# Kernel optimization log

Hardware: AMD Instinct MI355X
Metric: run time of the kernel (lower is better)

## Reference

```python
import jax, jax.numpy as jnp
import numpy as np

N_NODES = 100000
N_EDGES = 1600000
IN_DIM = 256
HEADS = 4
OUT_DIM = 32
NEG_SLOPE = 0.2


def setup_inputs() -> dict:
    key = jax.random.key(0)
    ks = jax.random.split(key, 6)
    x = jax.random.normal(ks[0], (N_NODES, IN_DIM), dtype=jnp.float32)
    # xavier-ish init scale for fc and attention vectors
    W = jax.random.normal(ks[1], (IN_DIM, HEADS * OUT_DIM), dtype=jnp.float32) * (1.0 / np.sqrt(IN_DIM))
    attn_l = jax.random.normal(ks[2], (HEADS, OUT_DIM), dtype=jnp.float32) * (1.0 / np.sqrt(OUT_DIM))
    attn_r = jax.random.normal(ks[3], (HEADS, OUT_DIM), dtype=jnp.float32) * (1.0 / np.sqrt(OUT_DIM))
    src = jax.random.randint(ks[4], (N_EDGES,), 0, N_NODES, dtype=jnp.int32)
    dst = jax.random.randint(ks[5], (N_EDGES,), 0, N_NODES, dtype=jnp.int32)
    return {"x": x, "W": W, "attn_l": attn_l, "attn_r": attn_r, "src": src, "dst": dst}


def reference(x, W, attn_l, attn_r, src, dst):
    N = x.shape[0]
    H, D = attn_l.shape
    # shared linear projection (feat_drop = 0)
    feat = (x @ W).reshape(N, H, D)                      # [N,H,D]
    el = jnp.sum(feat * attn_l, axis=-1)                 # [N,H]
    er = jnp.sum(feat * attn_r, axis=-1)                 # [N,H]
    e = jax.nn.leaky_relu(el[src] + er[dst], NEG_SLOPE)  # [E,H]
    # edge softmax over incoming edges of each destination node
    m = jax.ops.segment_max(e, dst, num_segments=N)      # [N,H]
    m = jnp.where(jnp.isfinite(m), m, 0.0)               # zero-in-degree guard
    ex = jnp.exp(e - m[dst])                             # [E,H]
    denom = jax.ops.segment_sum(ex, dst, num_segments=N) # [N,H]
    a = ex / jnp.maximum(denom[dst], 1e-9)               # [E,H] (attn_drop = 0)
    # weighted scatter-add aggregation
    out = jax.ops.segment_sum(a[:, :, None] * feat[src], dst, num_segments=N)  # [N,H,D]
    # head mean (the .mean(1) in GAT1.forward)
    return out.mean(axis=1)                              # [N,D]
```

## Files before the change

### kernel.cpp

```cpp
#include <hip/hip_runtime.h>
#include <math.h>

#define NN 100000
#define NE 1600000
#define IN_DIM 256
#define HD 128
#define NEG_SLOPE 0.2f

#define B1SH 9
#define NPB (1 << B1SH)
#define NB1 ((NN + NPB - 1) / NPB)
#define SC_BLOCKS ((NE / 4 + 1023) / 1024)

typedef __attribute__((ext_vector_type(8))) __bf16 bf16x8;
typedef __attribute__((ext_vector_type(4))) float floatx4;

__device__ inline unsigned short f2bf(float f) {
    unsigned int b = __float_as_uint(f);
    b += 0x7fffu + ((b >> 16) & 1u);
    return (unsigned short)(b >> 16);
}
__device__ inline unsigned int pk(float lo, float hi) {
    return (unsigned int)f2bf(lo) | ((unsigned int)f2bf(hi) << 16);
}
__device__ inline float bflo(unsigned int u) { return __uint_as_float(u << 16); }
__device__ inline float bfhi(unsigned int u) { return __uint_as_float(u & 0xffff0000u); }
__device__ inline float lrelu(float v) { return (v > 0.f) ? v : v * NEG_SLOPE; }

__global__ __launch_bounds__(256) void prep_w_kernel(const float* __restrict__ W,
                                                     unsigned int* __restrict__ wswz) {
    int g = blockIdx.x * 256 + threadIdx.x;
    int lane = g & 63;
    int t = (g >> 6) & 7;
    int c = g >> 9;
    int sub = lane & 15, quad = lane >> 4;
    int n = t * 16 + sub;
    int kbase = c * 32 + quad * 8;
    unsigned int ob = (unsigned int)g * 4;
#pragma unroll
    for (int i = 0; i < 4; ++i) {
        float lo = W[(size_t)(kbase + 2 * i) * HD + n];
        float hi = W[(size_t)(kbase + 2 * i + 1) * HD + n];
        wswz[ob + i] = pk(lo, hi);
    }
}

__global__ __launch_bounds__(256, 4) void gemm_kernel(const float* __restrict__ x,
                                                      const uint4* __restrict__ wswz,
                                                      const float* __restrict__ attn_l,
                                                      const float* __restrict__ attn_r,
                                                      unsigned short* __restrict__ featb,
                                                      float* __restrict__ el,
                                                      float* __restrict__ er) {
    const int tid = threadIdx.x;
    const int lane = tid & 63, wv = tid >> 6;
    const int sub = lane & 15, quad = lane >> 4;
    const int row0 = blockIdx.x * 64 + wv * 16;

    int m = row0 + sub;
    if (m >= NN) m = NN - 1;
    const float* xp = x + (size_t)m * IN_DIM + quad * 8;

    bf16x8 af[8];
#pragma unroll
    for (int h = 0; h < 2; ++h) {
        float4 raw[4][2];
#pragma unroll
        for (int c = 0; c < 4; ++c) {
            raw[c][0] = *(const float4*)(xp + (h * 4 + c) * 32);
            raw[c][1] = *(const float4*)(xp + (h * 4 + c) * 32 + 4);
        }
#pragma unroll
        for (int c = 0; c < 4; ++c) {
            uint4 au;
            au.x = pk(raw[c][0].x, raw[c][0].y);
            au.y = pk(raw[c][0].z, raw[c][0].w);
            au.z = pk(raw[c][1].x, raw[c][1].y);
            au.w = pk(raw[c][1].z, raw[c][1].w);
            af[h * 4 + c] = __builtin_bit_cast(bf16x8, au);
        }
    }

    floatx4 acc[8];
#pragma unroll
    for (int t = 0; t < 8; ++t) acc[t] = (floatx4){0.f, 0.f, 0.f, 0.f};

#pragma unroll
    for (int c = 0; c < 8; ++c) {
        uint4 bu[8];
#pragma unroll
        for (int t = 0; t < 8; ++t) bu[t] = wswz[(c * 8 + t) * 64 + lane];
#pragma unroll
        for (int t = 0; t < 8; ++t) {
            bf16x8 bfr = __builtin_bit_cast(bf16x8, bu[t]);
            acc[t] = __builtin_amdgcn_mfma_f32_16x16x32_bf16(af[c], bfr, acc[t], 0, 0, 0);
        }
    }

    float al[8], ar[8];
#pragma unroll
    for (int t = 0; t < 8; ++t) {
        al[t] = attn_l[t * 16 + sub];
        ar[t] = attn_r[t * 16 + sub];
    }

#pragma unroll
    for (int r = 0; r < 4; ++r) {
        int row = row0 + quad * 4 + r;
        uint4 fv;
        fv.x = pk(acc[0][r], acc[1][r]);
        fv.y = pk(acc[2][r], acc[3][r]);
        fv.z = pk(acc[4][r], acc[5][r]);
        fv.w = pk(acc[6][r], acc[7][r]);
        float pl[4], pr[4];
#pragma unroll
        for (int hh = 0; hh < 4; ++hh) {
            pl[hh] = acc[2 * hh][r] * al[2 * hh] + acc[2 * hh + 1][r] * al[2 * hh + 1];
            pr[hh] = acc[2 * hh][r] * ar[2 * hh] + acc[2 * hh + 1][r] * ar[2 * hh + 1];
        }
#pragma unroll
        for (int o = 1; o < 16; o <<= 1) {
#pragma unroll
            for (int hh = 0; hh < 4; ++hh) {
                pl[hh] += __shfl_xor(pl[hh], o);
                pr[hh] += __shfl_xor(pr[hh], o);
            }
        }
        if (row < NN) {
            *(uint4*)(featb + (size_t)row * HD + sub * 8) = fv;
            if (sub < 4) {
                float vl = (sub == 0) ? pl[0] : (sub == 1) ? pl[1] : (sub == 2) ? pl[2] : pl[3];
                float vr = (sub == 0) ? pr[0] : (sub == 1) ? pr[1] : (sub == 2) ? pr[2] : pr[3];
                el[row * 4 + sub] = vl;
                er[row * 4 + sub] = vr;
            }
        }
    }
}

__global__ __launch_bounds__(256) void precount_kernel(const int4* __restrict__ dst4,
                                                       int* __restrict__ gbcnt) {
    __shared__ int cnt[NB1];
    int t = threadIdx.x;
    for (int i = t; i < NB1; i += 256) cnt[i] = 0;
    __syncthreads();
    int base4 = blockIdx.x * 1024;
#pragma unroll
    for (int k = 0; k < 4; ++k) {
        int gi = base4 + k * 256 + t;
        if (gi < NE / 4) {
            int4 d = dst4[gi];
            atomicAdd(&cnt[d.x >> B1SH], 1);
            atomicAdd(&cnt[d.y >> B1SH], 1);
            atomicAdd(&cnt[d.z >> B1SH], 1);
            atomicAdd(&cnt[d.w >> B1SH], 1);
        }
    }
    __syncthreads();
    for (int i = t; i < NB1; i += 256)
        if (cnt[i]) atomicAdd(&gbcnt[i], cnt[i]);
}

__global__ __launch_bounds__(256) void bscan_kernel(const int* __restrict__ gbcnt,
                                                    int* __restrict__ regstart,
                                                    int* __restrict__ gcursor,
                                                    int* __restrict__ offs) {
    __shared__ int sh[256];
    int t = threadIdx.x;
    int v = (t < NB1) ? gbcnt[t] : 0;
    sh[t] = v;
    __syncthreads();
    for (int o = 1; o < 256; o <<= 1) {
        int a = (t >= o) ? sh[t - o] : 0;
        __syncthreads();
        sh[t] += a;
        __syncthreads();
    }
    int excl = sh[t] - v;
    if (t < NB1) {
        regstart[t] = excl;
        gcursor[t] = excl;
    }
    if (t == 0) {
        regstart[NB1] = NE;
        offs[NN] = NE;
    }
}

__global__ __launch_bounds__(256) void scatter_kernel(const int4* __restrict__ src4,
                                                      const int4* __restrict__ dst4,
                                                      int* __restrict__ gcursor,
                                                      unsigned int* __restrict__ pkd) {
    __shared__ int cnt[NB1];
    __shared__ int gbase[NB1];
    int t = threadIdx.x;
    for (int i = t; i < NB1; i += 256) cnt[i] = 0;
    __syncthreads();

    int base4 = blockIdx.x * 1024;
    unsigned int pkv[16];
    unsigned int brk[16];
#pragma unroll
    for (int k = 0; k < 4; ++k) {
        int gi = base4 + k * 256 + t;
        bool ok = gi < NE / 4;
        int gic = ok ? gi : 0;
        int4 s = src4[gic];
        int4 d = dst4[gic];
        int dd[4] = {d.x, d.y, d.z, d.w};
        int ss[4] = {s.x, s.y, s.z, s.w};
#pragma unroll
        for (int j4 = 0; j4 < 4; ++j4) {
            int e = k * 4 + j4;
            if (ok) {
                int b = dd[j4] >> B1SH;
                int r = atomicAdd(&cnt[b], 1);
                brk[e] = ((unsigned int)b << 12) | (unsigned int)r;
                pkv[e] = ((unsigned int)(dd[j4] & (NPB - 1)) << 17) | (unsigned int)ss[j4];
            } else {
                brk[e] = 0xFFFFFFFFu;
            }
        }
    }
    __syncthreads();
    for (int i = t; i < NB1; i += 256)
        gbase[i] = cnt[i] ? atomicAdd(&gcursor[i], cnt[i]) : 0;
    __syncthreads();
#pragma unroll
    for (int e = 0; e < 16; ++e) {
        if (brk[e] != 0xFFFFFFFFu) {
            int b = brk[e] >> 12;
            int r = brk[e] & 0xFFF;
            pkd[gbase[b] + r] = pkv[e];
        }
    }
}

__global__ __launch_bounds__(256) void build_kernel(const unsigned int* __restrict__ pkd,
                                                    const int* __restrict__ regstart,
                                                    int* __restrict__ offs,
                                                    int* __restrict__ csr_src) {
    __shared__ int fcnt[NPB];
    __shared__ int foffs[NPB];
    __shared__ int ssc[256];
    int b = blockIdx.x, t = threadIdx.x;
    int rs = regstart[b], re = regstart[b + 1];
    int n = re - rs;

    for (int i = t; i < NPB; i += 256) fcnt[i] = 0;
    __syncthreads();
    for (int i = t; i < n; i += 256) {
        unsigned int v = pkd[rs + i];
        atomicAdd(&fcnt[v >> 17], 1);
    }
    __syncthreads();
    int a0 = fcnt[2 * t], a1 = fcnt[2 * t + 1];
    int s = a0 + a1;
    ssc[t] = s;
    __syncthreads();
    for (int o = 1; o < 256; o <<= 1) {
        int u = (t >= o) ? ssc[t - o] : 0;
        __syncthreads();
        ssc[t] += u;
        __syncthreads();
    }
    int excl = ssc[t] - s;
    foffs[2 * t] = excl;
    foffs[2 * t + 1] = excl + a0;
    __syncthreads();
#pragma unroll
    for (int q = 0; q < 2; ++q) {
        int j = t + q * 256;
        int node = b * NPB + j;
        if (node < NN) offs[node] = rs + foffs[j];
    }
    for (int i = t; i < NPB; i += 256) fcnt[i] = 0;
    __syncthreads();
    int i = t;
    for (; i + 768 < n; i += 1024) {
        unsigned int v0 = pkd[rs + i];
        unsigned int v1 = pkd[rs + i + 256];
        unsigned int v2 = pkd[rs + i + 512];
        unsigned int v3 = pkd[rs + i + 768];
        int j0 = v0 >> 17, j1 = v1 >> 17, j2 = v2 >> 17, j3 = v3 >> 17;
        int r0 = atomicAdd(&fcnt[j0], 1);
        int r1 = atomicAdd(&fcnt[j1], 1);
        int r2 = atomicAdd(&fcnt[j2], 1);
        int r3 = atomicAdd(&fcnt[j3], 1);
        csr_src[rs + foffs[j0] + r0] = (int)(v0 & 0x1FFFFu);
        csr_src[rs + foffs[j1] + r1] = (int)(v1 & 0x1FFFFu);
        csr_src[rs + foffs[j2] + r2] = (int)(v2 & 0x1FFFFu);
        csr_src[rs + foffs[j3] + r3] = (int)(v3 & 0x1FFFFu);
    }
    for (; i < n; i += 256) {
        unsigned int v = pkd[rs + i];
        int j = v >> 17;
        int r = atomicAdd(&fcnt[j], 1);
        csr_src[rs + foffs[j] + r] = (int)(v & 0x1FFFFu);
    }
}

#define CH 32
__global__ __launch_bounds__(256) void aggregate_kernel(const uint4* __restrict__ featu4,
                                                        const float4* __restrict__ el4,
                                                        const float4* __restrict__ er4,
                                                        const int* __restrict__ offs,
                                                        const int* __restrict__ csr_src,
                                                        float* __restrict__ out) {
    __shared__ int    s_sv[4][4][CH];
    __shared__ float4 s_a4[4][4][CH];

    const int tid = threadIdx.x;
    const int lane = tid & 63, wv = tid >> 6;
    const int g = lane >> 4, sub = lane & 15;
    const int node = blockIdx.x * 16 + wv * 4 + g;
    const int beg = offs[node], end = offs[node + 1];

    const float4 erv = er4[node];
    float4 sm = make_float4(0.f, 0.f, 0.f, 0.f);
    float acc[8];
#pragma unroll
    for (int i = 0; i < 8; ++i) acc[i] = 0.f;

    for (int c0 = beg; c0 < end; c0 += CH) {
        int cnt = end - c0;
        if (cnt > CH) cnt = CH;
#pragma unroll
        for (int t = 0; t < 2; ++t) {
            int slot = sub + t * 16;
            if (slot < cnt) {
                int s = csr_src[c0 + slot];
                float4 e = el4[s];
                float4 w;
                w.x = __expf(lrelu(e.x + erv.x));
                w.y = __expf(lrelu(e.y + erv.y));
                w.z = __expf(lrelu(e.z + erv.z));
                w.w = __expf(lrelu(e.w + erv.w));
                sm.x += w.x; sm.y += w.y; sm.z += w.z; sm.w += w.w;
                s_sv[wv][g][slot] = s;
                s_a4[wv][g][slot] = w;
            }
        }
        int j = 0;
        for (; j + 4 <= cnt; j += 4) {
            int s0 = s_sv[wv][g][j + 0];
            int s1 = s_sv[wv][g][j + 1];
            int s2 = s_sv[wv][g][j + 2];
            int s3 = s_sv[wv][g][j + 3];
            uint4 u0 = featu4[(size_t)s0 * 16 + sub];
            uint4 u1 = featu4[(size_t)s1 * 16 + sub];
            uint4 u2 = featu4[(size_t)s2 * 16 + sub];
            uint4 u3 = featu4[(size_t)s3 * 16 + sub];
            float4 w0 = s_a4[wv][g][j + 0];
            float4 w1 = s_a4[wv][g][j + 1];
            float4 w2 = s_a4[wv][g][j + 2];
            float4 w3 = s_a4[wv][g][j + 3];
            acc[0] = fmaf(w0.x, bflo(u0.x), acc[0]); acc[1] = fmaf(w0.x, bfhi(u0.x), acc[1]);
            acc[2] = fmaf(w0.y, bflo(u0.y), acc[2]); acc[3] = fmaf(w0.y, bfhi(u0.y), acc[3]);
            acc[4] = fmaf(w0.z, bflo(u0.z), acc[4]); acc[5] = fmaf(w0.z, bfhi(u0.z), acc[5]);
            acc[6] = fmaf(w0.w, bflo(u0.w), acc[6]); acc[7] = fmaf(w0.w, bfhi(u0.w), acc[7]);
            acc[0] = fmaf(w1.x, bflo(u1.x), acc[0]); acc[1] = fmaf(w1.x, bfhi(u1.x), acc[1]);
            acc[2] = fmaf(w1.y, bflo(u1.y), acc[2]); acc[3] = fmaf(w1.y, bfhi(u1.y), acc[3]);
            acc[4] = fmaf(w1.z, bflo(u1.z), acc[4]); acc[5] = fmaf(w1.z, bfhi(u1.z), acc[5]);
            acc[6] = fmaf(w1.w, bflo(u1.w), acc[6]); acc[7] = fmaf(w1.w, bfhi(u1.w), acc[7]);
            acc[0] = fmaf(w2.x, bflo(u2.x), acc[0]); acc[1] = fmaf(w2.x, bfhi(u2.x), acc[1]);
            acc[2] = fmaf(w2.y, bflo(u2.y), acc[2]); acc[3] = fmaf(w2.y, bfhi(u2.y), acc[3]);
            acc[4] = fmaf(w2.z, bflo(u2.z), acc[4]); acc[5] = fmaf(w2.z, bfhi(u2.z), acc[5]);
            acc[6] = fmaf(w2.w, bflo(u2.w), acc[6]); acc[7] = fmaf(w2.w, bfhi(u2.w), acc[7]);
            acc[0] = fmaf(w3.x, bflo(u3.x), acc[0]); acc[1] = fmaf(w3.x, bfhi(u3.x), acc[1]);
            acc[2] = fmaf(w3.y, bflo(u3.y), acc[2]); acc[3] = fmaf(w3.y, bfhi(u3.y), acc[3]);
            acc[4] = fmaf(w3.z, bflo(u3.z), acc[4]); acc[5] = fmaf(w3.z, bfhi(u3.z), acc[5]);
            acc[6] = fmaf(w3.w, bflo(u3.w), acc[6]); acc[7] = fmaf(w3.w, bfhi(u3.w), acc[7]);
        }
        for (; j < cnt; ++j) {
            int s = s_sv[wv][g][j];
            uint4 u = featu4[(size_t)s * 16 + sub];
            float4 w = s_a4[wv][g][j];
            acc[0] = fmaf(w.x, bflo(u.x), acc[0]); acc[1] = fmaf(w.x, bfhi(u.x), acc[1]);
            acc[2] = fmaf(w.y, bflo(u.y), acc[2]); acc[3] = fmaf(w.y, bfhi(u.y), acc[3]);
            acc[4] = fmaf(w.z, bflo(u.z), acc[4]); acc[5] = fmaf(w.z, bfhi(u.z), acc[5]);
            acc[6] = fmaf(w.w, bflo(u.w), acc[6]); acc[7] = fmaf(w.w, bfhi(u.w), acc[7]);
        }
    }

#pragma unroll
    for (int o = 1; o < 16; o <<= 1) {
        sm.x += __shfl_xor(sm.x, o);
        sm.y += __shfl_xor(sm.y, o);
        sm.z += __shfl_xor(sm.z, o);
        sm.w += __shfl_xor(sm.w, o);
    }
    float ix = 1.f / fmaxf(sm.x, 1e-9f);
    float iy = 1.f / fmaxf(sm.y, 1e-9f);
    float iz = 1.f / fmaxf(sm.z, 1e-9f);
    float iw = 1.f / fmaxf(sm.w, 1e-9f);
    float ox = 0.25f * (acc[0] * ix + acc[2] * iy + acc[4] * iz + acc[6] * iw);
    float oy = 0.25f * (acc[1] * ix + acc[3] * iy + acc[5] * iz + acc[7] * iw);
    out[node * 32 + sub]      = ox;
    out[node * 32 + 16 + sub] = oy;
}

extern "C" void kernel_launch(void* const* d_in, const int* in_sizes, int n_in,
                              void* d_out, int out_size, void* d_ws, size_t ws_size,
                              hipStream_t stream) {
    const float* x      = (const float*)d_in[0];
    const float* W      = (const float*)d_in[1];
    const float* attn_l = (const float*)d_in[2];
    const float* attn_r = (const float*)d_in[3];
    const int*   src    = (const int*)d_in[4];
    const int*   dst    = (const int*)d_in[5];
    float* out = (float*)d_out;

    char* p = (char*)d_ws;
    auto alloc = [&](size_t bytes) -> void* {
        void* r = (void*)p;
        p += (bytes + 255) & ~(size_t)255;
        return r;
    };
    unsigned short* featb = (unsigned short*)alloc((size_t)NN * HD * 2);
    unsigned int*   wswz  = (unsigned int*)alloc(4096 * 16);
    float* el      = (float*)alloc((size_t)NN * 4 * 4);
    float* er      = (float*)alloc((size_t)NN * 4 * 4);
    int*   offs    = (int*)alloc((size_t)(NN + 1) * 4);
    unsigned int* pkd = (unsigned int*)alloc((size_t)NE * 4);
    int*   csr     = (int*)alloc((size_t)NE * 4);
    int*   gbcnt   = (int*)alloc((size_t)NB1 * 4);
    int*   regstart= (int*)alloc((size_t)(NB1 + 1) * 4);
    int*   gcursor = (int*)alloc((size_t)NB1 * 4);

    hipMemsetAsync(gbcnt, 0, (size_t)NB1 * 4, stream);

    prep_w_kernel<<<16, 256, 0, stream>>>(W, wswz);
    gemm_kernel<<<(NN + 63) / 64, 256, 0, stream>>>(x, (const uint4*)wswz, attn_l, attn_r,
                                                    featb, el, er);
    precount_kernel<<<SC_BLOCKS, 256, 0, stream>>>((const int4*)dst, gbcnt);
    bscan_kernel<<<1, 256, 0, stream>>>(gbcnt, regstart, gcursor, offs);
    scatter_kernel<<<SC_BLOCKS, 256, 0, stream>>>((const int4*)src, (const int4*)dst,
                                                  gcursor, pkd);
    build_kernel<<<NB1, 256, 0, stream>>>(pkd, regstart, offs, csr);
    aggregate_kernel<<<NN / 16, 256, 0, stream>>>((const uint4*)featb, (const float4*)el,
                                                  (const float4*)er, offs, csr, out);
}
```

Baseline: 303.6 us.

## Sort nodes by in-degree for aggregation and unroll gathers by eight with padding

Build a degree histogram during CSR construction, scan it, and fill a permutation that groups nodes by in-degree. The aggregate kernel then processes nodes in that order so that the four node groups sharing a wavefront have similar edge counts, which reduces divergence and load imbalance. The gather loop is padded to multiples of eight, with zero weights and index zero in the unused slots, and issues eight feature loads at once for more memory-level parallelism. A launch-bounds occupancy hint is also added. The cost is two extra small kernels, some wasted padded loads, and scattered output writes.

```diff
diff --git a/kernel.cpp b/kernel.cpp
--- a/kernel.cpp
+++ b/kernel.cpp
@@ -11,6 +11,7 @@
 #define NPB (1 << B1SH)
 #define NB1 ((NN + NPB - 1) / NPB)
 #define SC_BLOCKS ((NE / 4 + 1023) / 1024)
+#define DBK 64
 
 typedef __attribute__((ext_vector_type(8))) __bf16 bf16x8;
 typedef __attribute__((ext_vector_type(4))) float floatx4;
@@ -239,15 +240,18 @@
 __global__ __launch_bounds__(256) void build_kernel(const unsigned int* __restrict__ pkd,
                                                     const int* __restrict__ regstart,
                                                     int* __restrict__ offs,
-                                                    int* __restrict__ csr_src) {
+                                                    int* __restrict__ csr_src,
+                                                    int* __restrict__ dcnt) {
     __shared__ int fcnt[NPB];
     __shared__ int foffs[NPB];
     __shared__ int ssc[256];
+    __shared__ int dh[DBK];
     int b = blockIdx.x, t = threadIdx.x;
     int rs = regstart[b], re = regstart[b + 1];
     int n = re - rs;
 
     for (int i = t; i < NPB; i += 256) fcnt[i] = 0;
+    if (t < DBK) dh[t] = 0;
     __syncthreads();
     for (int i = t; i < n; i += 256) {
         unsigned int v = pkd[rs + i];
@@ -255,6 +259,11 @@
     }
     __syncthreads();
     int a0 = fcnt[2 * t], a1 = fcnt[2 * t + 1];
+    {
+        int node0 = b * NPB + 2 * t;
+        if (node0 < NN)     atomicAdd(&dh[a0 < DBK ? a0 : DBK - 1], 1);
+        if (node0 + 1 < NN) atomicAdd(&dh[a1 < DBK ? a1 : DBK - 1], 1);
+    }
     int s = a0 + a1;
     ssc[t] = s;
     __syncthreads();
@@ -268,6 +277,7 @@
     foffs[2 * t] = excl;
     foffs[2 * t + 1] = excl + a0;
     __syncthreads();
+    if (t < DBK && dh[t]) atomicAdd(&dcnt[t], dh[t]);
 #pragma unroll
     for (int q = 0; q < 2; ++q) {
         int j = t + q * 256;
@@ -300,20 +310,54 @@
     }
 }
 
+__global__ void degscan_kernel(const int* __restrict__ dcnt, int* __restrict__ dcur) {
+    int t = threadIdx.x;
+    int v = dcnt[t];
+    int s = v;
+#pragma unroll
+    for (int o = 1; o < 64; o <<= 1) {
+        int u = __shfl_up(s, o);
+        if (t >= o) s += u;
+    }
+    dcur[t] = s - v;
+}
+
+__global__ __launch_bounds__(256) void permfill_kernel(const int* __restrict__ offs,
+                                                       int* __restrict__ dcur,
+                                                       int* __restrict__ perm) {
+    __shared__ int c[DBK], base[DBK];
+    int t = threadIdx.x;
+    if (t < DBK) c[t] = 0;
+    __syncthreads();
+    int n = blockIdx.x * 256 + t;
+    int d = 0, r = 0;
+    bool ok = n < NN;
+    if (ok) {
+        d = offs[n + 1] - offs[n];
+        if (d > DBK - 1) d = DBK - 1;
+        r = atomicAdd(&c[d], 1);
+    }
+    __syncthreads();
+    if (t < DBK) base[t] = c[t] ? atomicAdd(&dcur[t], c[t]) : 0;
+    __syncthreads();
+    if (ok) perm[base[d] + r] = n;
+}
+
 #define CH 32
-__global__ __launch_bounds__(256) void aggregate_kernel(const uint4* __restrict__ featu4,
-                                                        const float4* __restrict__ el4,
-                                                        const float4* __restrict__ er4,
-                                                        const int* __restrict__ offs,
-                                                        const int* __restrict__ csr_src,
-                                                        float* __restrict__ out) {
+__global__ __launch_bounds__(256, 4) void aggregate_kernel(const uint4* __restrict__ featu4,
+                                                           const float4* __restrict__ el4,
+                                                           const float4* __restrict__ er4,
+                                                           const int* __restrict__ offs,
+                                                           const int* __restrict__ csr_src,
+                                                           const int* __restrict__ perm,
+                                                           float* __restrict__ out) {
     __shared__ int    s_sv[4][4][CH];
     __shared__ float4 s_a4[4][4][CH];
 
     const int tid = threadIdx.x;
     const int lane = tid & 63, wv = tid >> 6;
     const int g = lane >> 4, sub = lane & 15;
-    const int node = blockIdx.x * 16 + wv * 4 + g;
+    const int node = perm[blockIdx.x * 16 + wv * 4 + g];
     const int beg = offs[node], end = offs[node + 1];
 
     const float4 erv = er4[node];
@@ -328,58 +372,43 @@
 #pragma unroll
         for (int t = 0; t < 2; ++t) {
             int slot = sub + t * 16;
+            int sv = 0;
+            float4 w = make_float4(0.f, 0.f, 0.f, 0.f);
             if (slot < cnt) {
-                int s = csr_src[c0 + slot];
-                float4 e = el4[s];
-                float4 w;
+                sv = csr_src[c0 + slot];
+                float4 e = el4[sv];
                 w.x = __expf(lrelu(e.x + erv.x));
                 w.y = __expf(lrelu(e.y + erv.y));
                 w.z = __expf(lrelu(e.z + erv.z));
                 w.w = __expf(lrelu(e.w + erv.w));
                 sm.x += w.x; sm.y += w.y; sm.z += w.z; sm.w += w.w;
-                s_sv[wv][g][slot] = s;
-                s_a4[wv][g][slot] = w;
             }
-        }
-        int j = 0;
-        for (; j + 4 <= cnt; j += 4) {
-            int s0 = s_sv[wv][g][j + 0];
-            int s1 = s_sv[wv][g][j + 1];
-            int s2 = s_sv[wv][g][j + 2];
-            int s3 = s_sv[wv][g][j + 3];
-            uint4 u0 = featu4[(size_t)s0 * 16 + sub];
-            uint4 u1 = featu4[(size_t)s1 * 16 + sub];
-            uint4 u2 = featu4[(size_t)s2 * 16 + sub];
-            uint4 u3 = featu4[(size_t)s3 * 16 + sub];
-            float4 w0 = s_a4[wv][g][j + 0];
-            float4 w1 = s_a4[wv][g][j + 1];
-            float4 w2 = s_a4[wv][g][j + 2];
-            float4 w3 = s_a4[wv][g][j + 3];
-            acc[0] = fmaf(w0.x, bflo(u0.x), acc[0]); acc[1] = fmaf(w0.x, bfhi(u0.x), acc[1]);
-            acc[2] = fmaf(w0.y, bflo(u0.y), acc[2]); acc[3] = fmaf(w0.y, bfhi(u0.y), acc[3]);
-            acc[4] = fmaf(w0.z, bflo(u0.z), acc[4]); acc[5] = fmaf(w0.z, bfhi(u0.z), acc[5]);
-            acc[6] = fmaf(w0.w, bflo(u0.w), acc[6]); acc[7] = fmaf(w0.w, bfhi(u0.w), acc[7]);
-            acc[0] = fmaf(w1.x, bflo(u1.x), acc[0]); acc[1] = fmaf(w1.x, bfhi(u1.x), acc[1]);
-            acc[2] = fmaf(w1.y, bflo(u1.y), acc[2]); acc[3] = fmaf(w1.y, bfhi(u1.y), acc[3]);
-            acc[4] = fmaf(w1.z, bflo(u1.z), acc[4]); acc[5] = fmaf(w1.z, bfhi(u1.z), acc[5]);
-            acc[6] = fmaf(w1.w, bflo(u1.w), acc[6]); acc[7] = fmaf(w1.w, bfhi(u1.w), acc[7]);
-            acc[0] = fmaf(w2.x, bflo(u2.x), acc[0]); acc[1] = fmaf(w2.x, bfhi(u2.x), acc[1]);
-            acc[2] = fmaf(w2.y, bflo(u2.y), acc[2]); acc[3] = fmaf(w2.y, bfhi(u2.y), acc[3]);
-            acc[4] = fmaf(w2.z, bflo(u2.z), acc[4]); acc[5] = fmaf(w2.z, bfhi(u2.z), acc[5]);
-            acc[6] = fmaf(w2.w, bflo(u2.w), acc[6]); acc[7] = fmaf(w2.w, bfhi(u2.w), acc[7]);
-            acc[0] = fmaf(w3.x, bflo(u3.x), acc[0]); acc[1] = fmaf(w3.x, bfhi(u3.x), acc[1]);
-            acc[2] = fmaf(w3.y, bflo(u3.y), acc[2]); acc[3] = fmaf(w3.y, bfhi(u3.y), acc[3]);
-            acc[4] = fmaf(w3.z, bflo(u3.z), acc[4]); acc[5] = fmaf(w3.z, bfhi(u3.z), acc[5]);
-            acc[6] = fmaf(w3.w, bflo(u3.w), acc[6]); acc[7] = fmaf(w3.w, bfhi(u3.w), acc[7]);
-        }
-        for (; j < cnt; ++j) {
-            int s = s_sv[wv][g][j];
-            uint4 u = featu4[(size_t)s * 16 + sub];
-            float4 w = s_a4[wv][g][j];
-            acc[0] = fmaf(w.x, bflo(u.x), acc[0]); acc[1] = fmaf(w.x, bfhi(u.x), acc[1]);
-            acc[2] = fmaf(w.y, bflo(u.y), acc[2]); acc[3] = fmaf(w.y, bfhi(u.y), acc[3]);
-            acc[4] = fmaf(w.z, bflo(u.z), acc[4]); acc[5] = fmaf(w.z, bfhi(u.z), acc[5]);
-            acc[6] = fmaf(w.w, bflo(u.w), acc[6]); acc[7] = fmaf(w.w, bfhi(u.w), acc[7]);
+            s_sv[wv][g][slot] = sv;
+            s_a4[wv][g][slot] = w;
+        }
+        int rounds = (cnt + 7) >> 3;
+        for (int jr = 0; jr < rounds; ++jr) {
+            int jb = jr << 3;
+            int sv[8];
+#pragma unroll
+            for (int e = 0; e < 8; ++e) sv[e] = s_sv[wv][g][jb + e];
+            uint4 u[8];
+#pragma unroll
+            for (int e = 0; e < 8; ++e) u[e] = featu4[(size_t)sv[e] * 16 + sub];
+            float4 w[8];
+#pragma unroll
+            for (int e = 0; e < 8; ++e) w[e] = s_a4[wv][g][jb + e];
+#pragma unroll
+            for (int e = 0; e < 8; ++e) {
+                acc[0] = fmaf(w[e].x, bflo(u[e].x), acc[0]);
+                acc[1] = fmaf(w[e].x, bfhi(u[e].x), acc[1]);
+                acc[2] = fmaf(w[e].y, bflo(u[e].y), acc[2]);
+                acc[3] = fmaf(w[e].y, bfhi(u[e].y), acc[3]);
+                acc[4] = fmaf(w[e].z, bflo(u[e].z), acc[4]);
+                acc[5] = fmaf(w[e].z, bfhi(u[e].z), acc[5]);
+                acc[6] = fmaf(w[e].w, bflo(u[e].w), acc[6]);
+                acc[7] = fmaf(w[e].w, bfhi(u[e].w), acc[7]);
+            }
         }
     }
 
@@ -427,8 +456,12 @@
     int*   gbcnt   = (int*)alloc((size_t)NB1 * 4);
     int*   regstart= (int*)alloc((size_t)(NB1 + 1) * 4);
     int*   gcursor = (int*)alloc((size_t)NB1 * 4);
+    int*   dcnt    = (int*)alloc((size_t)DBK * 4);
+    int*   dcur    = (int*)alloc((size_t)DBK * 4);
+    int*   perm    = (int*)alloc((size_t)NN * 4);
 
     hipMemsetAsync(gbcnt, 0, (size_t)NB1 * 4, stream);
+    hipMemsetAsync(dcnt, 0, (size_t)DBK * 4, stream);
 
     prep_w_kernel<<<16, 256, 0, stream>>>(W, wswz);
     gemm_kernel<<<(NN + 63) / 64, 256, 0, stream>>>(x, (const uint4*)wswz, attn_l, attn_r,
@@ -437,7 +470,9 @@
     bscan_kernel<<<1, 256, 0, stream>>>(gbcnt, regstart, gcursor, offs);
     scatter_kernel<<<SC_BLOCKS, 256, 0, stream>>>((const int4*)src, (const int4*)dst,
                                                   gcursor, pkd);
-    build_kernel<<<NB1, 256, 0, stream>>>(pkd, regstart, offs, csr);
+    build_kernel<<<NB1, 256, 0, stream>>>(pkd, regstart, offs, csr, dcnt);
+    degscan_kernel<<<1, 64, 0, stream>>>(dcnt, dcur);
+    permfill_kernel<<<(NN + 255) / 256, 256, 0, stream>>>(offs, dcur, perm);
     aggregate_kernel<<<NN / 16, 256, 0, stream>>>((const uint4*)featb, (const float4*)el,
-                                                  (const float4*)er, offs, csr, out);
-}
+                                                  (const float4*)er, offs, csr, perm, out);
+}
```

Result: slower. 319.6 us (+5.3%).
